# Performance work log

Hardware: AMD Instinct MI355X
Metric: run time of the kernel (lower is better)

Reference implementation:

```python
import jax, jax.numpy as jnp
import numpy as np

HEADS = 8
EPS = 1e-5

def setup_inputs() -> dict:
    key = jax.random.key(0)
    k1, k2, k3 = jax.random.split(key, 3)
    b, c, n = 4, 512, 2048
    x = jax.random.normal(k1, (b, c, n), dtype=jnp.float32)
    g = jnp.ones((c,), dtype=jnp.float32)
    w_qkv = jax.random.normal(k2, (3 * c, c), dtype=jnp.float32) * (1.0 / np.sqrt(c))
    w_out = jax.random.normal(k3, (c, c), dtype=jnp.float32) * (1.0 / np.sqrt(c))
    b_out = jnp.zeros((c,), dtype=jnp.float32)
    return {"x": x, "g": g, "w_qkv": w_qkv, "w_out": w_out, "b_out": b_out}

def reference(x, g, w_qkv, w_out, b_out):
    b, c, n = x.shape
    h = HEADS
    d = c // h
    scale = d ** -0.5
    # channel LayerNorm (biased variance), scale g, no bias
    mean = jnp.mean(x, axis=1, keepdims=True)
    var = jnp.var(x, axis=1, keepdims=True)
    xn = (x - mean) * jax.lax.rsqrt(var + EPS) * g[None, :, None]
    # 1x1 conv == channel matmul: (3c, c) x (b, c, n) -> (b, 3c, n)
    qkv = jnp.einsum('oc,bcn->bon', w_qkv, xn)
    q, k, v = jnp.split(qkv, 3, axis=1)
    # b (h d) n -> b h d n
    q = q.reshape(b, h, d, n) * scale
    k = k.reshape(b, h, d, n)
    v = v.reshape(b, h, d, n)
    sim = jnp.einsum('bhdi,bhdj->bhij', q, k)  # [b,h,n,n]
    attn = jax.nn.softmax(sim, axis=-1)
    out = jnp.einsum('bhij,bhdj->bhid', attn, v)  # [b,h,n,d]
    out = out.transpose(0, 1, 3, 2).reshape(b, h * d, n)  # b (h d) n
    out = jnp.einsum('oc,bcn->bon', w_out, out) + b_out[None, :, None]
    return out
```

## Files before the change

kernel.cpp:

```cpp
#include <hip/hip_runtime.h>
#include <hip/hip_bf16.h>

#define B_ 4
#define C_ 512
#define N_ 2048
#define H_ 8
#define D_ 64
#define O3_ 1536
#define SPLIT 2
#define JTN 16

typedef __bf16 bf16x8 __attribute__((ext_vector_type(8)));
typedef float f32x4 __attribute__((ext_vector_type(4)));
typedef unsigned short ushort_t;

#define QSCALE 0.1803368801111137f

__device__ inline ushort_t f2b(float f) {
    __hip_bfloat16 h = __float2bfloat16(f);
    return *reinterpret_cast<ushort_t*>(&h);
}
__device__ inline float b2f(ushort_t u) {
    unsigned v = ((unsigned)u) << 16;
    return *reinterpret_cast<float*>(&v);
}

__device__ inline void gload16(const ushort_t* g, ushort_t* l) {
    __builtin_amdgcn_global_load_lds(
        (const __attribute__((address_space(1))) unsigned int*)g,
        (__attribute__((address_space(3))) unsigned int*)l, 16, 0, 0);
}

__global__ __launch_bounds__(256) void k_pre(const float* __restrict__ x,
                                             const float* __restrict__ g,
                                             ushort_t* __restrict__ xnT,
                                             const float* __restrict__ wqkv,
                                             const float* __restrict__ wout,
                                             ushort_t* __restrict__ wqkv_b,
                                             ushort_t* __restrict__ wout_b) {
    if (blockIdx.x >= 256) {
        int i = (blockIdx.x - 256) * 256 + threadIdx.x;
        float4 a = reinterpret_cast<const float4*>(wqkv)[i];
        ushort4 o;
        o.x = f2b(a.x); o.y = f2b(a.y); o.z = f2b(a.z); o.w = f2b(a.w);
        reinterpret_cast<ushort4*>(wqkv_b)[i] = o;
        if (i < 65536) {
            float4 c = reinterpret_cast<const float4*>(wout)[i];
            ushort4 oc;
            oc.x = f2b(c.x); oc.y = f2b(c.y); oc.z = f2b(c.z); oc.w = f2b(c.w);
            reinterpret_cast<ushort4*>(wout_b)[i] = oc;
        }
        return;
    }

    int bid = blockIdx.x;
    int b  = bid >> 6;
    int j0 = (bid & 63) * 32;
    int t  = threadIdx.x;

    __shared__ float s_red[8][32];
    __shared__ float s_red2[8][32];
    __shared__ float s_mean[32], s_rstd[32];
    __shared__ float s_g[C_];
    __shared__ __align__(16) ushort_t s_t[32][C_ + 2];

    for (int i = t; i < C_; i += 256) s_g[i] = g[i];

    int jl = t & 31, cg = t >> 5;
    const float* xb = x + (size_t)b * C_ * N_;

    float sum = 0.f, sq = 0.f;
#pragma unroll 4
    for (int c = cg * 64; c < cg * 64 + 64; ++c) {
        float v = xb[(size_t)c * N_ + j0 + jl];
        sum += v; sq += v * v;
    }
    s_red[cg][jl] = sum; s_red2[cg][jl] = sq;
    __syncthreads();
    if (t < 32) {
        float s = 0.f, q = 0.f;
#pragma unroll
        for (int i = 0; i < 8; ++i) { s += s_red[i][t]; q += s_red2[i][t]; }
        float mean = s * (1.0f / C_);
        float var  = q * (1.0f / C_) - mean * mean;
        s_mean[t] = mean;
        s_rstd[t] = rsqrtf(var + 1e-5f);
    }
    __syncthreads();

    for (int it = 0; it < 64; ++it) {
        int c = it * 8 + cg;
        float v  = xb[(size_t)c * N_ + j0 + jl];
        float xn = (v - s_mean[jl]) * s_rstd[jl] * s_g[c];
        s_t[jl][c] = f2b(xn);
    }
    __syncthreads();

    for (int jr = 0; jr < 32; ++jr) {
        unsigned val = *reinterpret_cast<const unsigned*>(&s_t[jr][t * 2]);
        *reinterpret_cast<unsigned*>(
            &xnT[((size_t)(b * N_ + j0 + jr)) * C_ + t * 2]) = val;
    }
}

template <int MODE>
__global__ __launch_bounds__(256) void k_gemm(const ushort_t* __restrict__ A,
                                              const ushort_t* __restrict__ Bt,
                                              ushort_t* __restrict__ qT,
                                              ushort_t* __restrict__ kT,
                                              ushort_t* __restrict__ vv,
                                              float* __restrict__ out,
                                              const float* __restrict__ b_out) {
    constexpr int M = (MODE == 0) ? O3_ : C_;
    constexpr int K = C_;
    constexpr int NMT = M / 128;

    int bid = blockIdx.x;
    int b   = bid / (NMT * 16);
    int rem = bid % (NMT * 16);
    int mt0 = (rem / 16) * 128;
    int nt0 = (rem % 16) * 128;

    int t = threadIdx.x;
    int w = t >> 6, lane = t & 63;
    int wm = (w >> 1) * 64, wn = (w & 1) * 64;
    int low = lane & 15, hi = lane >> 4;

    __shared__ __align__(16) ushort_t sA[128][64];
    __shared__ __align__(16) ushort_t sB[128][64];

    const ushort_t* Bb = Bt + (size_t)b * N_ * K;

    int srow = lane >> 3;
    int sseg = (lane & 7) ^ srow;
    const ushort_t* Ag = A  + (size_t)(mt0 + w * 32 + srow) * K + sseg * 8;
    const ushort_t* Bg = Bb + (size_t)(nt0 + w * 32 + srow) * K + sseg * 8;

    f32x4 acc[4][4] = {};

    for (int k0 = 0; k0 < K; k0 += 64) {
#pragma unroll
        for (int i = 0; i < 4; ++i) {
            gload16(Ag + (size_t)(i * 8) * K + k0, &sA[w * 32 + i * 8][0]);
            gload16(Bg + (size_t)(i * 8) * K + k0, &sB[w * 32 + i * 8][0]);
        }
        asm volatile("s_waitcnt vmcnt(0)" ::: "memory");
        __syncthreads();
#pragma unroll
        for (int kk = 0; kk < 64; kk += 32) {
            bf16x8 af[4], bfr[4];
#pragma unroll
            for (int mt = 0; mt < 4; ++mt) {
                int cseg = ((kk >> 3) + hi) ^ (low & 7);
                af[mt] = *reinterpret_cast<const bf16x8*>(
                    &sA[wm + mt * 16 + low][cseg * 8]);
            }
#pragma unroll
            for (int nt = 0; nt < 4; ++nt) {
                int cseg = ((kk >> 3) + hi) ^ (low & 7);
                bfr[nt] = *reinterpret_cast<const bf16x8*>(
                    &sB[wn + nt * 16 + low][cseg * 8]);
            }
#pragma unroll
            for (int mt = 0; mt < 4; ++mt)
#pragma unroll
                for (int nt = 0; nt < 4; ++nt)
                    acc[mt][nt] = __builtin_amdgcn_mfma_f32_16x16x32_bf16(
                        af[mt], bfr[nt], acc[mt][nt], 0, 0, 0);
        }
        __syncthreads();
    }

#pragma unroll
    for (int mt = 0; mt < 4; ++mt)
#pragma unroll
        for (int nt = 0; nt < 4; ++nt) {
            int m0 = mt0 + wm + mt * 16 + hi * 4;
            int j  = nt0 + wn + nt * 16 + low;
            if constexpr (MODE == 0) {
                if (m0 < 512) {
                    ushort4 pk;
                    pk.x = f2b(acc[mt][nt][0] * QSCALE);
                    pk.y = f2b(acc[mt][nt][1] * QSCALE);
                    pk.z = f2b(acc[mt][nt][2] * QSCALE);
                    pk.w = f2b(acc[mt][nt][3] * QSCALE);
                    *reinterpret_cast<ushort4*>(
                        &qT[(((size_t)(b * H_ + (m0 >> 6)) * N_) + j) * D_ +
                            (m0 & 63)]) = pk;
                } else if (m0 < 1024) {
                    int mm = m0 - 512;
                    ushort4 pk;
                    pk.x = f2b(acc[mt][nt][0]);
                    pk.y = f2b(acc[mt][nt][1]);
                    pk.z = f2b(acc[mt][nt][2]);
                    pk.w = f2b(acc[mt][nt][3]);
                    *reinterpret_cast<ushort4*>(
                        &kT[(((size_t)(b * H_ + (mm >> 6)) * N_) + j) * D_ +
                            (mm & 63)]) = pk;
                } else {
                    int mm0 = m0 - 1024;
#pragma unroll
                    for (int r = 0; r < 4; ++r)
                        vv[(((size_t)(b * H_ + (mm0 >> 6)) * D_) +
                            ((mm0 & 63) + r)) * N_ + j] = f2b(acc[mt][nt][r]);
                }
            } else {
#pragma unroll
                for (int r = 0; r < 4; ++r)
                    out[((size_t)(b * C_ + m0 + r)) * N_ + j] =
                        acc[mt][nt][r] + b_out[m0 + r];
            }
        }
}

__global__ __launch_bounds__(512, 4) void k_attn(const ushort_t* __restrict__ qT,
                                                 const ushort_t* __restrict__ kT,
                                                 const ushort_t* __restrict__ vv,
                                                 ushort_t* __restrict__ O0,
                                                 ushort_t* __restrict__ O1,
                                                 float* __restrict__ Lp) {
    int bid  = blockIdx.x;
    int sbid = ((bid & 7) << 6) | (bid >> 3);
    int it256 = sbid & 7;
    int s     = (sbid >> 3) & 1;
    int h     = (sbid >> 4) & 7;
    int b     = sbid >> 7;
    int i0    = it256 * 256;
    int t = threadIdx.x, w = t >> 6, lane = t & 63;
    int low = lane & 15, hi = lane >> 4;

    __shared__ ushort_t sK[2][64][64];
    __shared__ ushort_t sV[2][64][64];
    __shared__ __align__(16) ushort_t sPT[256][72];

    const ushort_t* qb = qT + ((size_t)(b * H_ + h)) * N_ * D_;
    const ushort_t* kb = kT + ((size_t)(b * H_ + h)) * N_ * D_;
    const ushort_t* vb = vv + ((size_t)(b * H_ + h)) * D_ * N_;

    int srow = lane >> 3;
    int sseg = (lane & 7) ^ srow;
    const ushort_t* kg = kb + (size_t)(w * 8 + srow) * D_ + sseg * 8;
    const ushort_t* vg = vb + (size_t)(w * 8 + srow) * N_ + sseg * 8;

    bf16x8 qf[2][2];
#pragma unroll
    for (int mt = 0; mt < 2; ++mt)
#pragma unroll
        for (int kx = 0; kx < 2; ++kx)
            qf[mt][kx] = *reinterpret_cast<const bf16x8*>(
                &qb[(size_t)(i0 + w * 32 + mt * 16 + low) * D_ + kx * 32 + hi * 8]);

    {
        int j0 = s * JTN * 64;
        gload16(kg + (size_t)j0 * D_, &sK[0][w * 8][0]);
        gload16(vg + j0,              &sV[0][w * 8][0]);
    }
    asm volatile("s_waitcnt vmcnt(0)" ::: "memory");
    __syncthreads();

    f32x4 oacc[2][4] = {};
    float lp0 = 0.f, lp1 = 0.f;
    int sw = (low & 7) * 8;

    int buf = 0;
    for (int jj = 0; jj < JTN; ++jj) {
        int j0c = (s * JTN + jj) * 64;

        if (jj + 1 < JTN) {
            int j0n = j0c + 64;
            gload16(kg + (size_t)j0n * D_, &sK[buf ^ 1][w * 8][0]);
            gload16(vg + j0n,              &sV[buf ^ 1][w * 8][0]);
        }

        f32x4 sacc[2][4] = {};
#pragma unroll
        for (int kx = 0; kx < 2; ++kx) {
            bf16x8 kfx[4];
#pragma unroll
            for (int nt = 0; nt < 4; ++nt)
                kfx[nt] = *reinterpret_cast<const bf16x8*>(
                    &sK[buf][nt * 16 + low][((kx * 4 + hi) * 8) ^ sw]);
#pragma unroll
            for (int mt = 0; mt < 2; ++mt)
#pragma unroll
                for (int nt = 0; nt < 4; ++nt)
                    sacc[mt][nt] = __builtin_amdgcn_mfma_f32_16x16x32_bf16(
                        kfx[nt], qf[mt][kx], sacc[mt][nt], 0, 0, 0);
        }

        bf16x8 vf[2][4];
#pragma unroll
        for (int kx = 0; kx < 2; ++kx)
#pragma unroll
            for (int dt = 0; dt < 4; ++dt)
                vf[kx][dt] = *reinterpret_cast<const bf16x8*>(
                    &sV[buf][dt * 16 + low][((kx * 4 + hi) * 8) ^ sw]);

#pragma unroll
        for (int mt = 0; mt < 2; ++mt) {
            int qrow = w * 32 + mt * 16 + low;
#pragma unroll
            for (int nt = 0; nt < 4; ++nt) {
                float p0 = __builtin_amdgcn_exp2f(sacc[mt][nt][0]);
                float p1 = __builtin_amdgcn_exp2f(sacc[mt][nt][1]);
                float p2 = __builtin_amdgcn_exp2f(sacc[mt][nt][2]);
                float p3 = __builtin_amdgcn_exp2f(sacc[mt][nt][3]);
                if (mt == 0) lp0 += (p0 + p1) + (p2 + p3);
                else         lp1 += (p0 + p1) + (p2 + p3);
                ushort4 pk;
                pk.x = f2b(p0); pk.y = f2b(p1); pk.z = f2b(p2); pk.w = f2b(p3);
                *reinterpret_cast<ushort4*>(&sPT[qrow][nt * 16 + hi * 4]) = pk;
            }
        }

#pragma unroll
        for (int kx = 0; kx < 2; ++kx) {
            bf16x8 ap0 = *reinterpret_cast<const bf16x8*>(
                &sPT[w * 32 + low][kx * 32 + hi * 8]);
            bf16x8 ap1 = *reinterpret_cast<const bf16x8*>(
                &sPT[w * 32 + 16 + low][kx * 32 + hi * 8]);
#pragma unroll
            for (int dt = 0; dt < 4; ++dt) {
                oacc[0][dt] = __builtin_amdgcn_mfma_f32_16x16x32_bf16(
                    ap0, vf[kx][dt], oacc[0][dt], 0, 0, 0);
                oacc[1][dt] = __builtin_amdgcn_mfma_f32_16x16x32_bf16(
                    ap1, vf[kx][dt], oacc[1][dt], 0, 0, 0);
            }
        }

        asm volatile("s_waitcnt vmcnt(0)" ::: "memory");
        __syncthreads();
        buf ^= 1;
    }

    lp0 += __shfl_xor(lp0, 16); lp0 += __shfl_xor(lp0, 32);
    lp1 += __shfl_xor(lp1, 16); lp1 += __shfl_xor(lp1, 32);

    float* lrow = Lp + ((size_t)((s * B_ + b) * H_ + h)) * N_ + i0 + w * 32;
    if (lane < 16) {
        lrow[low]      = lp0;
        lrow[16 + low] = lp1;
    }

    ushort_t* op = (s == 0 ? O0 : O1) +
                   ((size_t)(b * N_ + i0 + w * 32)) * C_ + h * D_;
#pragma unroll
    for (int mt = 0; mt < 2; ++mt)
#pragma unroll
        for (int dt = 0; dt < 4; ++dt)
#pragma unroll
            for (int r = 0; r < 4; ++r)
                op[(size_t)(mt * 16 + hi * 4 + r) * C_ + dt * 16 + low] =
                    f2b(oacc[mt][dt][r]);
}

__global__ __launch_bounds__(256) void k_comb(const ushort_t* __restrict__ O1,
                                              const float* __restrict__ Lp,
                                              ushort_t* __restrict__ attnT) {
    int tid = blockIdx.x * 256 + threadIdx.x;
    int d4 = (tid & 15) * 4;
    int i  = (tid >> 4) & (N_ - 1);
    int bh = tid >> 15;
    int b = bh >> 3, h = bh & 7;
    size_t idx = ((size_t)(b * N_ + i)) * C_ + h * D_ + d4;
    ushort4 a0 = *reinterpret_cast<const ushort4*>(&attnT[idx]);
    ushort4 a1 = *reinterpret_cast<const ushort4*>(&O1[idx]);
    float l = Lp[(size_t)bh * N_ + i] + Lp[(size_t)(B_ * H_ + bh) * N_ + i];
    float linv = 1.0f / l;
    ushort4 o;
    o.x = f2b((b2f(a0.x) + b2f(a1.x)) * linv);
    o.y = f2b((b2f(a0.y) + b2f(a1.y)) * linv);
    o.z = f2b((b2f(a0.z) + b2f(a1.z)) * linv);
    o.w = f2b((b2f(a0.w) + b2f(a1.w)) * linv);
    *reinterpret_cast<ushort4*>(&attnT[idx]) = o;
}

extern "C" void kernel_launch(void* const* d_in, const int* in_sizes, int n_in,
                              void* d_out, int out_size, void* d_ws, size_t ws_size,
                              hipStream_t stream) {
    const float* x    = (const float*)d_in[0];
    const float* g    = (const float*)d_in[1];
    const float* wqkv = (const float*)d_in[2];
    const float* wout = (const float*)d_in[3];
    const float* bout = (const float*)d_in[4];
    float* out = (float*)d_out;

    char* ws = (char*)d_ws;
    ushort_t* xnT    = (ushort_t*)(ws);
    ushort_t* qT     = (ushort_t*)(ws + (size_t)8  * 1024 * 1024);
    ushort_t* kT     = (ushort_t*)(ws + (size_t)16 * 1024 * 1024);
    ushort_t* vv     = (ushort_t*)(ws + (size_t)24 * 1024 * 1024);
    ushort_t* attnT  = (ushort_t*)(ws + (size_t)32 * 1024 * 1024);
    ushort_t* wqkv_b = (ushort_t*)(ws + (size_t)40 * 1024 * 1024);
    ushort_t* wout_b = (ushort_t*)(ws + (size_t)42 * 1024 * 1024);
    float*    Lp     = (float*)   (ws + (size_t)43 * 1024 * 1024);

    k_pre<<<dim3(1024), dim3(256), 0, stream>>>(
        x, g, xnT, wqkv, wout, wqkv_b, wout_b);
    k_gemm<0><<<dim3(B_ * (O3_ / 128) * (N_ / 128)), dim3(256), 0, stream>>>(
        wqkv_b, xnT, qT, kT, vv, nullptr, nullptr);
    k_attn<<<dim3(B_ * H_ * (N_ / 256) * SPLIT), dim3(512), 0, stream>>>(
        qT, kT, vv, attnT, xnT, Lp);
    k_comb<<<dim3(4096), dim3(256), 0, stream>>>(xnT, Lp, attnT);
    k_gemm<1><<<dim3(B_ * (C_ / 128) * (N_ / 128)), dim3(256), 0, stream>>>(
        wout_b, attnT, nullptr, nullptr, nullptr, out, bout);
}
```

Baseline: 99.76 us.

## Keep softmax probabilities in registers via permlane swaps, widen per-wave query tile

After: 105.9 us. 6.2% more time.

```diff
diff --git a/kernel.cpp b/kernel.cpp
--- a/kernel.cpp
+++ b/kernel.cpp
@@ -23,6 +23,15 @@
 __device__ inline float b2f(ushort_t u) {
     unsigned v = ((unsigned)u) << 16;
     return *reinterpret_cast<float*>(&v);
+}
+__device__ inline unsigned pkbf(float a, float b) {
+    return (unsigned)f2b(a) | ((unsigned)f2b(b) << 16);
+}
+__device__ inline void pl32swap(unsigned& a, unsigned& b) {
+    asm volatile("v_permlane32_swap_b32 %0, %1" : "+v"(a), "+v"(b));
+}
+__device__ inline void pl16swap(unsigned& a, unsigned& b) {
+    asm volatile("v_permlane16_swap_b32 %0, %1" : "+v"(a), "+v"(b));
 }
 
 __device__ inline void gload16(const ushort_t* g, ushort_t* l) {
@@ -213,7 +222,7 @@
         }
 }
 
-__global__ __launch_bounds__(512, 4) void k_attn(const ushort_t* __restrict__ qT,
+__global__ __launch_bounds__(256, 2) void k_attn(const ushort_t* __restrict__ qT,
                                                  const ushort_t* __restrict__ kT,
                                                  const ushort_t* __restrict__ vv,
                                                  ushort_t* __restrict__ O0,
@@ -231,7 +240,6 @@
 
     __shared__ ushort_t sK[2][64][64];
     __shared__ ushort_t sV[2][64][64];
-    __shared__ __align__(16) ushort_t sPT[256][72];
 
     const ushort_t* qb = qT + ((size_t)(b * H_ + h)) * N_ * D_;
     const ushort_t* kb = kT + ((size_t)(b * H_ + h)) * N_ * D_;
@@ -239,40 +247,42 @@
 
     int srow = lane >> 3;
     int sseg = (lane & 7) ^ srow;
-    const ushort_t* kg = kb + (size_t)(w * 8 + srow) * D_ + sseg * 8;
-    const ushort_t* vg = vb + (size_t)(w * 8 + srow) * N_ + sseg * 8;
-
-    bf16x8 qf[2][2];
-#pragma unroll
-    for (int mt = 0; mt < 2; ++mt)
+    const ushort_t* kg = kb + (size_t)(w * 16 + srow) * D_ + sseg * 8;
+    const ushort_t* vg = vb + (size_t)(w * 16 + srow) * N_ + sseg * 8;
+
+    bf16x8 qf[4][2];
+#pragma unroll
+    for (int mt = 0; mt < 4; ++mt)
 #pragma unroll
         for (int kx = 0; kx < 2; ++kx)
             qf[mt][kx] = *reinterpret_cast<const bf16x8*>(
-                &qb[(size_t)(i0 + w * 32 + mt * 16 + low) * D_ + kx * 32 + hi * 8]);
+                &qb[(size_t)(i0 + w * 64 + mt * 16 + low) * D_ + kx * 32 + hi * 8]);
 
     {
         int j0 = s * JTN * 64;
-        gload16(kg + (size_t)j0 * D_, &sK[0][w * 8][0]);
-        gload16(vg + j0,              &sV[0][w * 8][0]);
+        gload16(kg + (size_t)j0 * D_,           &sK[0][w * 16][0]);
+        gload16(kg + (size_t)(j0 + 8) * D_,     &sK[0][w * 16 + 8][0]);
+        gload16(vg + j0,                        &sV[0][w * 16][0]);
+        gload16(vg + (size_t)8 * N_ + j0,       &sV[0][w * 16 + 8][0]);
     }
     asm volatile("s_waitcnt vmcnt(0)" ::: "memory");
     __syncthreads();
 
-    f32x4 oacc[2][4] = {};
-    float lp0 = 0.f, lp1 = 0.f;
+    f32x4 oacc[4][4] = {};
+    float lp[4] = {};
     int sw = (low & 7) * 8;
 
     int buf = 0;
     for (int jj = 0; jj < JTN; ++jj) {
-        int j0c = (s * JTN + jj) * 64;
-
         if (jj + 1 < JTN) {
-            int j0n = j0c + 64;
-            gload16(kg + (size_t)j0n * D_, &sK[buf ^ 1][w * 8][0]);
-            gload16(vg + j0n,              &sV[buf ^ 1][w * 8][0]);
-        }
-
-        f32x4 sacc[2][4] = {};
+            int j0n = (s * JTN + jj + 1) * 64;
+            gload16(kg + (size_t)j0n * D_,       &sK[buf ^ 1][w * 16][0]);
+            gload16(kg + (size_t)(j0n + 8) * D_, &sK[buf ^ 1][w * 16 + 8][0]);
+            gload16(vg + j0n,                    &sV[buf ^ 1][w * 16][0]);
+            gload16(vg + (size_t)8 * N_ + j0n,   &sV[buf ^ 1][w * 16 + 8][0]);
+        }
+
+        f32x4 sacc[4][4] = {};
 #pragma unroll
         for (int kx = 0; kx < 2; ++kx) {
             bf16x8 kfx[4];
@@ -281,7 +291,7 @@
                 kfx[nt] = *reinterpret_cast<const bf16x8*>(
                     &sK[buf][nt * 16 + low][((kx * 4 + hi) * 8) ^ sw]);
 #pragma unroll
-            for (int mt = 0; mt < 2; ++mt)
+            for (int mt = 0; mt < 4; ++mt)
 #pragma unroll
                 for (int nt = 0; nt < 4; ++nt)
                     sacc[mt][nt] = __builtin_amdgcn_mfma_f32_16x16x32_bf16(
@@ -297,34 +307,31 @@
                     &sV[buf][dt * 16 + low][((kx * 4 + hi) * 8) ^ sw]);
 
 #pragma unroll
-        for (int mt = 0; mt < 2; ++mt) {
-            int qrow = w * 32 + mt * 16 + low;
-#pragma unroll
-            for (int nt = 0; nt < 4; ++nt) {
-                float p0 = __builtin_amdgcn_exp2f(sacc[mt][nt][0]);
-                float p1 = __builtin_amdgcn_exp2f(sacc[mt][nt][1]);
-                float p2 = __builtin_amdgcn_exp2f(sacc[mt][nt][2]);
-                float p3 = __builtin_amdgcn_exp2f(sacc[mt][nt][3]);
-                if (mt == 0) lp0 += (p0 + p1) + (p2 + p3);
-                else         lp1 += (p0 + p1) + (p2 + p3);
-                ushort4 pk;
-                pk.x = f2b(p0); pk.y = f2b(p1); pk.z = f2b(p2); pk.w = f2b(p3);
-                *reinterpret_cast<ushort4*>(&sPT[qrow][nt * 16 + hi * 4]) = pk;
-            }
-        }
-
-#pragma unroll
-        for (int kx = 0; kx < 2; ++kx) {
-            bf16x8 ap0 = *reinterpret_cast<const bf16x8*>(
-                &sPT[w * 32 + low][kx * 32 + hi * 8]);
-            bf16x8 ap1 = *reinterpret_cast<const bf16x8*>(
-                &sPT[w * 32 + 16 + low][kx * 32 + hi * 8]);
-#pragma unroll
-            for (int dt = 0; dt < 4; ++dt) {
-                oacc[0][dt] = __builtin_amdgcn_mfma_f32_16x16x32_bf16(
-                    ap0, vf[kx][dt], oacc[0][dt], 0, 0, 0);
-                oacc[1][dt] = __builtin_amdgcn_mfma_f32_16x16x32_bf16(
-                    ap1, vf[kx][dt], oacc[1][dt], 0, 0, 0);
+        for (int mt = 0; mt < 4; ++mt) {
+            float p[4][4];
+#pragma unroll
+            for (int nt = 0; nt < 4; ++nt)
+#pragma unroll
+                for (int r = 0; r < 4; ++r) {
+                    p[nt][r] = __builtin_amdgcn_exp2f(sacc[mt][nt][r]);
+                    lp[mt] += p[nt][r];
+                }
+#pragma unroll
+            for (int kx = 0; kx < 2; ++kx) {
+                unsigned a0 = pkbf(p[2 * kx][0],     p[2 * kx][1]);
+                unsigned a1 = pkbf(p[2 * kx][2],     p[2 * kx][3]);
+                unsigned b0 = pkbf(p[2 * kx + 1][0], p[2 * kx + 1][1]);
+                unsigned b1 = pkbf(p[2 * kx + 1][2], p[2 * kx + 1][3]);
+                pl32swap(a0, b0);
+                pl16swap(a0, b0);
+                pl32swap(a1, b1);
+                pl16swap(a1, b1);
+                unsigned tw[4] = {a0, a1, b0, b1};
+                bf16x8 pb = *reinterpret_cast<const bf16x8*>(tw);
+#pragma unroll
+                for (int dt = 0; dt < 4; ++dt)
+                    oacc[mt][dt] = __builtin_amdgcn_mfma_f32_16x16x32_bf16(
+                        vf[kx][dt], pb, oacc[mt][dt], 0, 0, 0);
             }
         }
 
@@ -333,25 +340,31 @@
         buf ^= 1;
     }
 
-    lp0 += __shfl_xor(lp0, 16); lp0 += __shfl_xor(lp0, 32);
-    lp1 += __shfl_xor(lp1, 16); lp1 += __shfl_xor(lp1, 32);
-
-    float* lrow = Lp + ((size_t)((s * B_ + b) * H_ + h)) * N_ + i0 + w * 32;
-    if (lane < 16) {
-        lrow[low]      = lp0;
-        lrow[16 + low] = lp1;
+#pragma unroll
+    for (int mt = 0; mt < 4; ++mt) {
+        lp[mt] += __shfl_xor(lp[mt], 16);
+        lp[mt] += __shfl_xor(lp[mt], 32);
+    }
+    float* lrow = Lp + ((size_t)((s * B_ + b) * H_ + h)) * N_ + i0 + w * 64;
+    if (hi == 0) {
+#pragma unroll
+        for (int mt = 0; mt < 4; ++mt) lrow[mt * 16 + low] = lp[mt];
     }
 
     ushort_t* op = (s == 0 ? O0 : O1) +
-                   ((size_t)(b * N_ + i0 + w * 32)) * C_ + h * D_;
-#pragma unroll
-    for (int mt = 0; mt < 2; ++mt)
-#pragma unroll
-        for (int dt = 0; dt < 4; ++dt)
-#pragma unroll
-            for (int r = 0; r < 4; ++r)
-                op[(size_t)(mt * 16 + hi * 4 + r) * C_ + dt * 16 + low] =
-                    f2b(oacc[mt][dt][r]);
+                   ((size_t)(b * N_ + i0 + w * 64)) * C_ + h * D_;
+#pragma unroll
+    for (int mt = 0; mt < 4; ++mt)
+#pragma unroll
+        for (int dt = 0; dt < 4; ++dt) {
+            ushort4 pk;
+            pk.x = f2b(oacc[mt][dt][0]);
+            pk.y = f2b(oacc[mt][dt][1]);
+            pk.z = f2b(oacc[mt][dt][2]);
+            pk.w = f2b(oacc[mt][dt][3]);
+            *reinterpret_cast<ushort4*>(
+                &op[(size_t)(mt * 16 + low) * C_ + dt * 16 + hi * 4]) = pk;
+        }
 }
 
 __global__ __launch_bounds__(256) void k_comb(const ushort_t* __restrict__ O1,
@@ -399,7 +412,7 @@
         x, g, xnT, wqkv, wout, wqkv_b, wout_b);
     k_gemm<0><<<dim3(B_ * (O3_ / 128) * (N_ / 128)), dim3(256), 0, stream>>>(
         wqkv_b, xnT, qT, kT, vv, nullptr, nullptr);
-    k_attn<<<dim3(B_ * H_ * (N_ / 256) * SPLIT), dim3(512), 0, stream>>>(
+    k_attn<<<dim3(B_ * H_ * (N_ / 256) * SPLIT), dim3(256), 0, stream>>>(
         qT, kT, vv, attnT, xnT, Lp);
     k_comb<<<dim3(4096), dim3(256), 0, stream>>>(xnT, Lp, attnT);
     k_gemm<1><<<dim3(B_ * (C_ / 128) * (N_ / 128)), dim3(256), 0, stream>>>(
```
